# Performance work log

Hardware: AMD Instinct MI355X
Metric: run time of the kernel (lower is better)

Reference implementation:

```python
import jax, jax.numpy as jnp
import numpy as np

FACTOR = 3.0  # maxval of the per-image std uniform draw


def setup_inputs() -> dict:
    key = jax.random.key(0)
    k1, k2 = jax.random.split(key)
    x = jax.random.uniform(k1, (64, 512, 512, 3), dtype=jnp.float32)
    stds = jax.random.uniform(k2, (64,), dtype=jnp.float32)  # uniform [0,1), scaled by FACTOR in reference
    return {"x": x, "stds": stds}


def reference(x, stds):
    # Faithful port of AddingGaussianBlur. Note the original has ys = tf.cast(xs, ...)
    # (a bug), so the kernel depends only on the column coordinate; we reproduce it.
    B, H, W, C = x.shape
    std = stds * FACTOR  # per-image std ~ Uniform(0, factor), shape [B]
    xs_row = jnp.arange(-1, 2, dtype=jnp.float32)          # [-1, 0, 1]
    xs = jnp.broadcast_to(xs_row[None, :], (3, 3))          # meshgrid xs (rows repeat)
    s = std[:, None, None]                                  # [B,1,1]
    # k = exp(-(xs^2 + ys^2)/(2 std^2)) / (2 pi std^2) with ys == xs
    k = jnp.exp(-(xs**2 + xs**2) / (2.0 * s**2)) / (2.0 * np.pi * s**2)  # [B,3,3]
    k = k / jnp.sum(k, axis=(1, 2), keepdims=True)
    # SAME zero-padded 3x3 cross-correlation, same kernel for all 3 channels,
    # per-sample kernel: expressed as weighted sum of 9 shifted views (fully batched).
    xpad = jnp.pad(x, ((0, 0), (1, 1), (1, 1), (0, 0)))
    out = jnp.zeros_like(x)
    for di in range(3):
        for dj in range(3):
            out = out + k[:, di, dj][:, None, None, None] * xpad[:, di:di + H, dj:dj + W, :]
    return out
```

## Files before the change

### kernel.cpp

```cpp
#include <hip/hip_runtime.h>
#include <math.h>


constexpr int Wd     = 512;
constexpr int Hd     = 512;
constexpr int Cd     = 3;
constexpr int ROWF   = Wd * Cd;
constexpr int TPB    = ROWF / 4;
constexpr int RPB    = 32;
constexpr int STRIPS = Hd / RPB;

using f4 = __attribute__((ext_vector_type(4))) float;

__device__ __forceinline__ f4 f4zero() { return (f4){0.f, 0.f, 0.f, 0.f}; }

__global__ __launch_bounds__(TPB) void gauss_strip_kernel(
    const float* __restrict__ x,
    const float* __restrict__ stds,
    float* __restrict__ out)
{
    __shared__ f4 cs[2][TPB + 2];

    const int t = threadIdx.x;
    const int s = blockIdx.x % STRIPS;
    const int b = blockIdx.x / STRIPS;

    const float sg = stds[b] * 3.0f;
    const float e  = expf(-1.0f / (sg * sg));
    const float w1 = 1.0f / (3.0f * (1.0f + 2.0f * e));
    const float w0 = e * w1;

    const size_t imgbase = (size_t)b * Hd * ROWF;
    const float* px = x   + imgbase + (size_t)t * 4;
    float*       po = out + imgbase + (size_t)t * 4;

    const int r0 = s * RPB;

    f4 ra = (r0 > 0) ? *(const f4*)(px + (size_t)(r0 - 1) * ROWF) : f4zero();
    f4 rb = *(const f4*)(px + (size_t)r0 * ROWF);
    f4 rc = *(const f4*)(px + (size_t)(r0 + 1) * ROWF);

    if (t == 0) {
        cs[0][0] = cs[0][TPB + 1] = f4zero();
        cs[1][0] = cs[1][TPB + 1] = f4zero();
    }

    #pragma unroll 2
    for (int j = r0; j < r0 + RPB; ++j) {
        f4 rn = (j + 2 < Hd) ? *(const f4*)(px + (size_t)(j + 2) * ROWF)
                             : f4zero();

        f4 m = ra + rb + rc;

        f4* buf = cs[j & 1];
        buf[t + 1] = m;
        __syncthreads();

        const f4 p = buf[t];
        const f4 n = buf[t + 2];

        f4 o;
        o.x = w1 * m.x + w0 * (p.y + m.w);
        o.y = w1 * m.y + w0 * (p.z + n.x);
        o.z = w1 * m.z + w0 * (p.w + n.y);
        o.w = w1 * m.w + w0 * (m.x + n.z);

        __builtin_nontemporal_store(o, (f4*)(po + (size_t)j * ROWF));

        ra = rb; rb = rc; rc = rn;
    }
}

extern "C" void kernel_launch(void* const* d_in, const int* in_sizes, int n_in,
                              void* d_out, int out_size, void* d_ws, size_t ws_size,
                              hipStream_t stream) {
    const float* x    = (const float*)d_in[0];
    const float* stds = (const float*)d_in[1];
    float* out        = (float*)d_out;

    const int nblocks = 64 * STRIPS;
    gauss_strip_kernel<<<nblocks, TPB, 0, stream>>>(x, stds, out);
}
```

Baseline: 346.6 us.

## Stage small row groups in LDS with halo and swizzle block order

Swaps the 32-row streaming strip, which paid a barrier per row, for blocks of 4 output rows. Each block loads 6 input rows (with halo) into LDS once, synchronises once, then computes all outputs from LDS. Block indices are swizzled across 8 groups to spread memory traffic. The exchange is more blocks and a 1.5x halo re-read of input rows in return for fewer barriers and more memory-level parallelism per thread.

Result: faster. 332.6 us (-4.0%).

```diff
diff --git a/kernel.cpp b/kernel.cpp
--- a/kernel.cpp
+++ b/kernel.cpp
@@ -7,57 +7,66 @@
 constexpr int Cd     = 3;
 constexpr int ROWF   = Wd * Cd;
 constexpr int TPB    = ROWF / 4;
-constexpr int RPB    = 32;
-constexpr int STRIPS = Hd / RPB;
+constexpr int G      = 4;
+constexpr int SR     = G + 2;
+constexpr int LROW   = ROWF + 8;
+constexpr int GP_IMG = Hd / G;
+constexpr int NB     = 64 * GP_IMG;
 
 using f4 = __attribute__((ext_vector_type(4))) float;
 
-__device__ __forceinline__ f4 f4zero() { return (f4){0.f, 0.f, 0.f, 0.f}; }
+__device__ __forceinline__ f4 f4z() { return (f4){0.f, 0.f, 0.f, 0.f}; }
 
-__global__ __launch_bounds__(TPB) void gauss_strip_kernel(
+__global__ __launch_bounds__(TPB) void gauss_stage_kernel(
     const float* __restrict__ x,
     const float* __restrict__ stds,
     float* __restrict__ out)
 {
-    __shared__ f4 cs[2][TPB + 2];
+    __shared__ float lds[SR * LROW];
 
     const int t = threadIdx.x;
-    const int s = blockIdx.x % STRIPS;
-    const int b = blockIdx.x / STRIPS;
+
+    const int bid = blockIdx.x;
+    const int swz = (bid & 7) * (NB / 8) + (bid >> 3);
+    const int b   = swz >> 7;
+    const int g   = swz & (GP_IMG - 1);
+    const int r0  = g * G;
 
     const float sg = stds[b] * 3.0f;
     const float e  = expf(-1.0f / (sg * sg));
     const float w1 = 1.0f / (3.0f * (1.0f + 2.0f * e));
     const float w0 = e * w1;
 
-    const size_t imgbase = (size_t)b * Hd * ROWF;
-    const float* px = x   + imgbase + (size_t)t * 4;
-    float*       po = out + imgbase + (size_t)t * 4;
+    const float* img = x + (size_t)b * Hd * ROWF;
 
-    const int r0 = s * RPB;
+    f4 st[SR];
+    #pragma unroll
+    for (int i = 0; i < SR; ++i) {
+        const int row = r0 - 1 + i;
+        st[i] = (row >= 0 && row < Hd)
+              ? *(const f4*)(img + (size_t)row * ROWF + 4 * t)
+              : f4z();
+    }
+    #pragma unroll
+    for (int i = 0; i < SR; ++i)
+        *(f4*)(&lds[i * LROW + 4 + 4 * t]) = st[i];
 
-    f4 ra = (r0 > 0) ? *(const f4*)(px + (size_t)(r0 - 1) * ROWF) : f4zero();
-    f4 rb = *(const f4*)(px + (size_t)r0 * ROWF);
-    f4 rc = *(const f4*)(px + (size_t)(r0 + 1) * ROWF);
+    if (t < SR)              *(f4*)(&lds[t * LROW]) = f4z();
+    else if (t < 2 * SR)     *(f4*)(&lds[(t - SR) * LROW + 4 + ROWF]) = f4z();
 
-    if (t == 0) {
-        cs[0][0] = cs[0][TPB + 1] = f4zero();
-        cs[1][0] = cs[1][TPB + 1] = f4zero();
-    }
+    __syncthreads();
 
-    #pragma unroll 2
-    for (int j = r0; j < r0 + RPB; ++j) {
-        f4 rn = (j + 2 < Hd) ? *(const f4*)(px + (size_t)(j + 2) * ROWF)
-                             : f4zero();
+    float* po = out + (size_t)b * Hd * ROWF + 4 * t;
 
-        f4 m = ra + rb + rc;
+    #pragma unroll
+    for (int j = 0; j < G; ++j) {
+        const float* b0 = &lds[(j + 0) * LROW + 4 * t];
+        const float* b1 = &lds[(j + 1) * LROW + 4 * t];
+        const float* b2 = &lds[(j + 2) * LROW + 4 * t];
 
-        f4* buf = cs[j & 1];
-        buf[t + 1] = m;
-        __syncthreads();
-
-        const f4 p = buf[t];
-        const f4 n = buf[t + 2];
+        f4 p = *(const f4*)(b0)     + *(const f4*)(b1)     + *(const f4*)(b2);
+        f4 m = *(const f4*)(b0 + 4) + *(const f4*)(b1 + 4) + *(const f4*)(b2 + 4);
+        f4 n = *(const f4*)(b0 + 8) + *(const f4*)(b1 + 8) + *(const f4*)(b2 + 8);
 
         f4 o;
         o.x = w1 * m.x + w0 * (p.y + m.w);
@@ -65,9 +74,7 @@
         o.z = w1 * m.z + w0 * (p.w + n.y);
         o.w = w1 * m.w + w0 * (m.x + n.z);
 
-        __builtin_nontemporal_store(o, (f4*)(po + (size_t)j * ROWF));
-
-        ra = rb; rb = rc; rc = rn;
+        __builtin_nontemporal_store(o, (f4*)(po + (size_t)(r0 + j) * ROWF));
     }
 }
 
@@ -78,6 +85,5 @@
     const float* stds = (const float*)d_in[1];
     float* out        = (float*)d_out;
 
-    const int nblocks = 64 * STRIPS;
-    gauss_strip_kernel<<<nblocks, TPB, 0, stream>>>(x, stds, out);
+    gauss_stage_kernel<<<NB, TPB, 0, stream>>>(x, stds, out);
 }
```
